# Performance work log

Hardware: AMD Instinct MI355X
Metric: run time of the kernel (lower is better)

## Reference

```python
import jax, jax.numpy as jnp
import numpy as np

B, S, D, E, K = 4, 4096, 1024, 8, 2


def setup_inputs() -> dict:
    key = jax.random.key(0)
    k0, k1, k2 = jax.random.split(key, 3)
    return {
        "x": jax.random.normal(k0, (B, S, D), dtype=jnp.float32),
        "gate_w": jax.random.normal(k1, (E, D), dtype=jnp.float32) * 0.02,   # torch Linear weight [out,in]
        "gate_b": jnp.zeros((E,), dtype=jnp.float32),
        "expert_w": jax.random.normal(k2, (E, D, D), dtype=jnp.float32) * 0.02,  # [E, out, in]
        "expert_b": jnp.zeros((E, D), dtype=jnp.float32),
    }


def reference(x, gate_w, gate_b, expert_w, expert_b):
    b, s, d = x.shape
    h = x.reshape(-1, d)                                   # [T, D], T = b*s
    # Router: gate linear -> softmax (float32) -> top-k -> renormalize
    router_logits = h @ gate_w.T + gate_b                  # [T, E]
    probs = jax.nn.softmax(router_logits.astype(jnp.float32), axis=-1)
    router_weights, selected_experts = jax.lax.top_k(probs, K)  # [T, K]
    router_weights = router_weights / router_weights.sum(axis=-1, keepdims=True)
    router_weights = router_weights.astype(h.dtype)
    # Combine weights per (token, expert): sum of top-k weights routed to each expert
    cw = (jax.nn.one_hot(selected_experts, E, dtype=h.dtype)
          * router_weights[..., None]).sum(axis=1)         # [T, E]
    # Dense-equivalent of gather-linear-scatter: every expert on every token,
    # then weighted combine (mathematically identical to the per-expert loop).
    expert_out = jnp.einsum('td,eod->teo', h, expert_w) + expert_b[None]  # [T, E, D]
    out = jnp.einsum('te,teo->to', cw, expert_out)         # [T, D]
    return out.reshape(b, s, d), router_logits, selected_experts
```

## Files before the change

### kernel.cpp

```cpp
#include <hip/hip_runtime.h>
#include <hip/hip_bf16.h>

#define T_TOK 16384
#define D_DIM 1024
#define E_EXP 8
#define NPAIR 28

#define BM 128
#define BN 128
#define BK 64

#define CNT_STRIDE 64

typedef __attribute__((ext_vector_type(4))) float f32x4;
typedef __attribute__((ext_vector_type(2))) float f32x2;
typedef __attribute__((ext_vector_type(8))) short bf16x8;
typedef __attribute__((ext_vector_type(4))) unsigned short u16x4;

static __device__ __forceinline__ unsigned short f2bf(float f) {
    unsigned int u = __float_as_uint(f);
    unsigned int r = 0x7FFFu + ((u >> 16) & 1u);
    return (unsigned short)((u + r) >> 16);
}

#define GLOAD_LDS16(gp, lp) \
    __builtin_amdgcn_global_load_lds( \
        (const __attribute__((address_space(1))) void*)(gp), \
        (__attribute__((address_space(3))) void*)(lp), 16, 0, 0)

__global__ __launch_bounds__(256) void convert_w_kernel(
    const float* __restrict__ w, unsigned short* __restrict__ o) {
    const int n4 = (E_EXP * D_DIM * D_DIM) / 4;
    for (int i = blockIdx.x * 256 + threadIdx.x; i < n4; i += gridDim.x * 256) {
        f32x4 v = ((const f32x4*)w)[i];
        u16x4 p;
        p[0] = f2bf(v[0]); p[1] = f2bf(v[1]); p[2] = f2bf(v[2]); p[3] = f2bf(v[3]);
        ((u16x4*)o)[i] = p;
    }
}

#define RTOK 64
__global__ __launch_bounds__(512) void router_kernel(
    const float* __restrict__ x, const float* __restrict__ gate_w,
    const float* __restrict__ gate_b, float* __restrict__ out_logits,
    float* __restrict__ out_sel, int* __restrict__ counts,
    int* __restrict__ pair_token, f32x2* __restrict__ pair_w,
    unsigned short* __restrict__ xbf) {
    __shared__ float gw[E_EXP][D_DIM];
    __shared__ float gb_s[E_EXP];
    __shared__ float logits_s[RTOK][E_EXP];
    __shared__ int   cnt_local[NPAIR];
    __shared__ int   gbase[NPAIR];
    __shared__ int   ent_p[RTOK];
    __shared__ int   ent_pos[RTOK];
    __shared__ f32x2 ent_w[RTOK];

    const int tid = threadIdx.x;
    for (int i = tid; i < E_EXP * D_DIM; i += 512) gw[0][i] = gate_w[i];
    if (tid < E_EXP) gb_s[tid] = gate_b[tid];
    if (tid < NPAIR) cnt_local[tid] = 0;
    __syncthreads();

    const int lane = tid & 63, wv = tid >> 6;
    for (int j = 0; j < RTOK / 8; ++j) {
        const int jt = wv * (RTOK / 8) + j;
        const int t = blockIdx.x * RTOK + jt;
        const float* xrow = x + (size_t)t * D_DIM;
        unsigned short* xbrow = xbf + (size_t)t * D_DIM;
        float acc[E_EXP] = {};
        #pragma unroll
        for (int c = 0; c < 4; ++c) {
            const int col = c * 256 + lane * 4;
            f32x4 xv = *(const f32x4*)(xrow + col);
            u16x4 pk;
            pk[0] = f2bf(xv[0]); pk[1] = f2bf(xv[1]); pk[2] = f2bf(xv[2]); pk[3] = f2bf(xv[3]);
            *(u16x4*)(xbrow + col) = pk;
            #pragma unroll
            for (int e = 0; e < E_EXP; ++e) {
                f32x4 gv = *(const f32x4*)(&gw[e][col]);
                acc[e] += xv[0] * gv[0] + xv[1] * gv[1] + xv[2] * gv[2] + xv[3] * gv[3];
            }
        }
        #pragma unroll
        for (int e = 0; e < E_EXP; ++e) {
            float v = acc[e];
            #pragma unroll
            for (int off = 32; off > 0; off >>= 1) v += __shfl_xor(v, off, 64);
            acc[e] = v;
        }
        if (lane == 0) {
            #pragma unroll
            for (int e = 0; e < E_EXP; ++e) logits_s[jt][e] = acc[e] + gb_s[e];
        }
    }
    __syncthreads();
    if (tid < RTOK) {
        const int t = blockIdx.x * RTOK + tid;
        float l[E_EXP], p[E_EXP];
        float m = -1e30f;
        #pragma unroll
        for (int e = 0; e < E_EXP; ++e) { l[e] = logits_s[tid][e]; m = fmaxf(m, l[e]); }
        float s = 0.f;
        #pragma unroll
        for (int e = 0; e < E_EXP; ++e) { p[e] = expf(l[e] - m); s += p[e]; }
        #pragma unroll
        for (int e = 0; e < E_EXP; ++e) p[e] /= s;
        int e0 = 0; float p0 = p[0];
        #pragma unroll
        for (int e = 1; e < E_EXP; ++e) if (p[e] > p0) { p0 = p[e]; e0 = e; }
        int e1 = -1; float p1 = -1e30f;
        #pragma unroll
        for (int e = 0; e < E_EXP; ++e) if (e != e0 && p[e] > p1) { p1 = p[e]; e1 = e; }
        float denom = p0 + p1;
        float w0 = p0 / denom, w1 = p1 / denom;
        out_sel[t * 2 + 0] = (float)e0;
        out_sel[t * 2 + 1] = (float)e1;
        int lo = min(e0, e1), hi = max(e0, e1);
        float wl = (e0 < e1) ? w0 : w1;
        float wh = (e0 < e1) ? w1 : w0;
        int pp = (lo * (15 - lo)) / 2 + (hi - lo - 1);
        int pos = atomicAdd(&cnt_local[pp], 1);
        ent_p[tid] = pp; ent_pos[tid] = pos;
        f32x2 wv2; wv2[0] = wl; wv2[1] = wh;
        ent_w[tid] = wv2;
    }
    __syncthreads();
    if (tid < NPAIR) gbase[tid] = atomicAdd(&counts[tid * CNT_STRIDE], cnt_local[tid]);
    if (tid < RTOK * E_EXP / 4) {
        f32x4 v = ((const f32x4*)&logits_s[0][0])[tid];
        ((f32x4*)(out_logits + (size_t)blockIdx.x * RTOK * E_EXP))[tid] = v;
    }
    __syncthreads();
    if (tid < RTOK) {
        int pp = ent_p[tid];
        int pos = gbase[pp] + ent_pos[tid];
        pair_token[pp * T_TOK + pos] = blockIdx.x * RTOK + tid;
        pair_w[pp * T_TOK + pos] = ent_w[tid];
    }
}

__global__ __launch_bounds__(256, 2) void moe_gemm_kernel(
    const unsigned short* __restrict__ xbf, const unsigned short* __restrict__ wbf,
    const float* __restrict__ expert_b, const int* __restrict__ counts,
    const int* __restrict__ pair_token, const f32x2* __restrict__ pair_w,
    float* __restrict__ out) {
    const int flat = blockIdx.x;
    const int cls = flat & 7;
    const int nt  = (flat >> 3) & 7;
    const int sup = flat >> 6;
    const int gidx = sup * 8 + cls;

    __shared__ int hdr[5];
    const int tid = threadIdx.x;
    if (tid < 64) {
        int c = (tid < NPAIR) ? counts[tid * CNT_STRIDE] : 0;
        int ntp = (c + BM - 1) >> 7;
        int s = ntp;
        #pragma unroll
        for (int off = 1; off < 64; off <<= 1) {
            int v = __shfl_up(s, off, 64);
            if (tid >= off) s += v;
        }
        int excl = s - ntp;
        bool mine = (tid < NPAIR) && (gidx >= excl) && (gidx < s);
        unsigned long long mb = __ballot(mine);
        int p = mb ? (__ffsll((long long)mb) - 1) : 0;
        int exclp = __shfl(excl, p, 64);
        int cp = __shfl(c, p, 64);
        if (tid == 0) {
            if (mb == 0) { hdr[0] = -1; }
            else {
                int lo = 0, q = p;
                while (q >= 7 - lo) { q -= 7 - lo; ++lo; }
                hdr[0] = lo; hdr[1] = lo + 1 + q;
                hdr[2] = (gidx - exclp) * BM; hdr[3] = cp; hdr[4] = p;
            }
        }
    }
    __syncthreads();
    const int lo = hdr[0];
    if (lo < 0) return;
    const int hi = hdr[1];
    const int m_base = hdr[2];
    const int cnt = hdr[3];
    const int p = hdr[4];
    const int n_base = nt * BN;

    __shared__ unsigned short As[BM * BK];
    __shared__ unsigned short B0s[BM * BK];
    __shared__ unsigned short B1s[BM * BK];
    __shared__ int tok_s[BM];
    __shared__ f32x2 w_s[BM];

    if (tid < BM) {
        int m = m_base + tid;
        int mc = (m < cnt) ? m : (cnt - 1);
        tok_s[tid] = pair_token[p * T_TOK + mc];
        w_s[tid]   = pair_w[p * T_TOK + mc];
    }
    __syncthreads();

    const int lane = tid & 63;
    const int w = tid >> 6;
    const int lr = lane & 15, lk = lane >> 4;
    const int wr = w >> 1, wc = w & 1;

    const int srow = lane >> 3;
    const int scol = 8 * ((lane & 7) ^ srow);
    const unsigned short* wb0 = wbf + ((size_t)lo << 20);
    const unsigned short* wb1 = wbf + ((size_t)hi << 20);
    const unsigned short* agp[4];
    const unsigned short* b0gp[4];
    const unsigned short* b1gp[4];
    int loff[4];
    #pragma unroll
    for (int i = 0; i < 4; ++i) {
        int R = i * 32 + w * 8 + srow;
        agp[i]  = xbf + (size_t)tok_s[R] * D_DIM + scol;
        b0gp[i] = wb0 + (size_t)(n_base + R) * D_DIM + scol;
        b1gp[i] = wb1 + (size_t)(n_base + R) * D_DIM + scol;
        loff[i] = (i * 32 + w * 8) * BK;
    }

    f32x4 acc0[4][4] = {};
    f32x4 acc1[4][4] = {};

    for (int k0 = 0; k0 < D_DIM; k0 += BK) {
        #pragma unroll
        for (int i = 0; i < 4; ++i) {
            GLOAD_LDS16(agp[i] + k0, &As[loff[i]]);
            GLOAD_LDS16(b0gp[i] + k0, &B0s[loff[i]]);
            GLOAD_LDS16(b1gp[i] + k0, &B1s[loff[i]]);
        }
        __syncthreads();
        #pragma unroll
        for (int kk = 0; kk < 2; ++kk) {
            bf16x8 a[4], b[4], c[4];
            #pragma unroll
            for (int m = 0; m < 4; ++m) {
                int R = wr * 64 + m * 16 + lr;
                int cb = (kk * 64 + lk * 16) ^ ((R & 7) << 4);
                a[m] = *(const bf16x8*)((const char*)As + R * 128 + cb);
            }
            #pragma unroll
            for (int n = 0; n < 4; ++n) {
                int R = wc * 64 + n * 16 + lr;
                int cb = (kk * 64 + lk * 16) ^ ((R & 7) << 4);
                b[n] = *(const bf16x8*)((const char*)B0s + R * 128 + cb);
            }
            #pragma unroll
            for (int m = 0; m < 4; ++m)
                #pragma unroll
                for (int n = 0; n < 4; ++n)
                    acc0[m][n] = __builtin_amdgcn_mfma_f32_16x16x32_bf16(a[m], b[n], acc0[m][n], 0, 0, 0);
            #pragma unroll
            for (int n = 0; n < 4; ++n) {
                int R = wc * 64 + n * 16 + lr;
                int cb = (kk * 64 + lk * 16) ^ ((R & 7) << 4);
                c[n] = *(const bf16x8*)((const char*)B1s + R * 128 + cb);
            }
            #pragma unroll
            for (int m = 0; m < 4; ++m)
                #pragma unroll
                for (int n = 0; n < 4; ++n)
                    acc1[m][n] = __builtin_amdgcn_mfma_f32_16x16x32_bf16(a[m], c[n], acc1[m][n], 0, 0, 0);
        }
        __syncthreads();
    }

    float blo[4], bhi[4];
    #pragma unroll
    for (int n = 0; n < 4; ++n) {
        int gn = n_base + wc * 64 + n * 16 + lr;
        blo[n] = expert_b[lo * D_DIM + gn];
        bhi[n] = expert_b[hi * D_DIM + gn];
    }
    #pragma unroll
    for (int m = 0; m < 4; ++m) {
        #pragma unroll
        for (int j = 0; j < 4; ++j) {
            int mi = wr * 64 + m * 16 + lk * 4 + j;
            if (m_base + mi >= cnt) continue;
            int tk = tok_s[mi];
            f32x2 wgt = w_s[mi];
            size_t obase = (size_t)tk * D_DIM + n_base + wc * 64 + lr;
            #pragma unroll
            for (int n = 0; n < 4; ++n)
                out[obase + n * 16] = wgt[0] * (acc0[m][n][j] + blo[n])
                                    + wgt[1] * (acc1[m][n][j] + bhi[n]);
        }
    }
}

extern "C" void kernel_launch(void* const* d_in, const int* in_sizes, int n_in,
                              void* d_out, int out_size, void* d_ws, size_t ws_size,
                              hipStream_t stream) {
    const float* x        = (const float*)d_in[0];
    const float* gate_w   = (const float*)d_in[1];
    const float* gate_b   = (const float*)d_in[2];
    const float* expert_w = (const float*)d_in[3];
    const float* expert_b = (const float*)d_in[4];

    float* out        = (float*)d_out;
    float* out_logits = out + (size_t)T_TOK * D_DIM;
    float* out_sel    = out_logits + (size_t)T_TOK * E_EXP;

    char* ws = (char*)d_ws;
    unsigned short* wbf = (unsigned short*)ws;
    unsigned short* xbf = (unsigned short*)(ws + 16777216);
    size_t off = 50331648;
    int*   counts     = (int*)(ws + off);
    int*   pair_token = (int*)(ws + off + 16384);
    f32x2* pair_w     = (f32x2*)(ws + off + 16384 + 1835008);

    hipMemsetAsync(counts, 0, NPAIR * CNT_STRIDE * sizeof(int), stream);

    convert_w_kernel<<<2048, 256, 0, stream>>>(expert_w, wbf);
    router_kernel<<<T_TOK / RTOK, 512, 0, stream>>>(x, gate_w, gate_b, out_logits,
                                                    out_sel, counts, pair_token,
                                                    pair_w, xbf);
    moe_gemm_kernel<<<20 * 64, 256, 0, stream>>>(xbf, wbf, expert_b, counts,
                                                 pair_token, pair_w, out);
}
```

Baseline: 134.7 us.

## Fuse weight conversion into router launch and double-buffer the MoE GEMM

The separate fp32-to-bf16 expert-weight conversion kernel is folded into the router launch as extra blocks, so conversion and routing run concurrently and one launch is removed. The grouped GEMM moves from 256 to 512 threads with an 8-wave 2x4 layout (smaller per-wave accumulator tiles) and double-buffered LDS. The next k-tile is prefetched while the current one computes, using explicit vmcnt waits, raw barriers and setprio around the MFMA bursts. LDS use doubles and occupancy drops to about one block per CU, and the hand-placed waitcnt/barrier scheme is fragile.

```diff
diff --git a/kernel.cpp b/kernel.cpp
--- a/kernel.cpp
+++ b/kernel.cpp
@@ -9,6 +9,7 @@
 #define BM 128
 #define BN 128
 #define BK 64
+#define NT_K (D_DIM / BK)
 
 #define CNT_STRIDE 64
 
@@ -28,24 +29,28 @@
         (const __attribute__((address_space(1))) void*)(gp), \
         (__attribute__((address_space(3))) void*)(lp), 16, 0, 0)
 
-__global__ __launch_bounds__(256) void convert_w_kernel(
-    const float* __restrict__ w, unsigned short* __restrict__ o) {
-    const int n4 = (E_EXP * D_DIM * D_DIM) / 4;
-    for (int i = blockIdx.x * 256 + threadIdx.x; i < n4; i += gridDim.x * 256) {
-        f32x4 v = ((const f32x4*)w)[i];
-        u16x4 p;
-        p[0] = f2bf(v[0]); p[1] = f2bf(v[1]); p[2] = f2bf(v[2]); p[3] = f2bf(v[3]);
-        ((u16x4*)o)[i] = p;
-    }
-}
-
 #define RTOK 64
-__global__ __launch_bounds__(512) void router_kernel(
+#define RBLK 256
+#define CBLK 128
+__global__ __launch_bounds__(512) void fused_router_kernel(
     const float* __restrict__ x, const float* __restrict__ gate_w,
     const float* __restrict__ gate_b, float* __restrict__ out_logits,
     float* __restrict__ out_sel, int* __restrict__ counts,
     int* __restrict__ pair_token, f32x2* __restrict__ pair_w,
-    unsigned short* __restrict__ xbf) {
+    unsigned short* __restrict__ xbf,
+    const float* __restrict__ expert_w, unsigned short* __restrict__ wbf) {
+    const int tid = threadIdx.x;
+    if (blockIdx.x >= RBLK) {
+        const int b = blockIdx.x - RBLK;
+        const int n4 = (E_EXP * D_DIM * D_DIM) / 4;
+        for (int i = b * 512 + tid; i < n4; i += CBLK * 512) {
+            f32x4 v = ((const f32x4*)expert_w)[i];
+            u16x4 p;
+            p[0] = f2bf(v[0]); p[1] = f2bf(v[1]); p[2] = f2bf(v[2]); p[3] = f2bf(v[3]);
+            ((u16x4*)wbf)[i] = p;
+        }
+        return;
+    }
     __shared__ float gw[E_EXP][D_DIM];
     __shared__ float gb_s[E_EXP];
     __shared__ float logits_s[RTOK][E_EXP];
@@ -55,7 +60,6 @@
     __shared__ int   ent_pos[RTOK];
     __shared__ f32x2 ent_w[RTOK];
 
-    const int tid = threadIdx.x;
     for (int i = tid; i < E_EXP * D_DIM; i += 512) gw[0][i] = gate_w[i];
     if (tid < E_EXP) gb_s[tid] = gate_b[tid];
     if (tid < NPAIR) cnt_local[tid] = 0;
@@ -139,7 +143,7 @@
     }
 }
 
-__global__ __launch_bounds__(256, 2) void moe_gemm_kernel(
+__global__ __launch_bounds__(512) void moe_gemm_kernel(
     const unsigned short* __restrict__ xbf, const unsigned short* __restrict__ wbf,
     const float* __restrict__ expert_b, const int* __restrict__ counts,
     const int* __restrict__ pair_token, const f32x2* __restrict__ pair_w,
@@ -186,9 +190,9 @@
     const int p = hdr[4];
     const int n_base = nt * BN;
 
-    __shared__ unsigned short As[BM * BK];
-    __shared__ unsigned short B0s[BM * BK];
-    __shared__ unsigned short B1s[BM * BK];
+    __shared__ unsigned short As[2][BM * BK];
+    __shared__ unsigned short B0s[2][BM * BK];
+    __shared__ unsigned short B1s[2][BM * BK];
     __shared__ int tok_s[BM];
     __shared__ f32x2 w_s[BM];
 
@@ -201,77 +205,89 @@
     __syncthreads();
 
     const int lane = tid & 63;
-    const int w = tid >> 6;
+    const int wv = tid >> 6;
+    const int wm = wv >> 2, wn = wv & 3;
     const int lr = lane & 15, lk = lane >> 4;
-    const int wr = w >> 1, wc = w & 1;
-
-    const int srow = lane >> 3;
-    const int scol = 8 * ((lane & 7) ^ srow);
+
+    const int r = tid >> 3;
+    const int swcol = 8 * ((tid & 7) ^ (r & 7));
     const unsigned short* wb0 = wbf + ((size_t)lo << 20);
     const unsigned short* wb1 = wbf + ((size_t)hi << 20);
-    const unsigned short* agp[4];
-    const unsigned short* b0gp[4];
-    const unsigned short* b1gp[4];
-    int loff[4];
+    const unsigned short* ag0  = xbf + (size_t)tok_s[r] * D_DIM + swcol;
+    const unsigned short* ag1  = xbf + (size_t)tok_s[64 + r] * D_DIM + swcol;
+    const unsigned short* b0g0 = wb0 + (size_t)(n_base + r) * D_DIM + swcol;
+    const unsigned short* b0g1 = wb0 + (size_t)(n_base + 64 + r) * D_DIM + swcol;
+    const unsigned short* b1g0 = wb1 + (size_t)(n_base + r) * D_DIM + swcol;
+    const unsigned short* b1g1 = wb1 + (size_t)(n_base + 64 + r) * D_DIM + swcol;
+    const int l0 = (wv * 64) * 8;
+    const int l1 = (512 + wv * 64) * 8;
+
+    f32x4 acc0[4][2] = {};
+    f32x4 acc1[4][2] = {};
+
+#define STAGE(buf, k0s) do { \
+        GLOAD_LDS16(ag0  + (k0s), &As[(buf)][l0]);  GLOAD_LDS16(ag1  + (k0s), &As[(buf)][l1]); \
+        GLOAD_LDS16(b0g0 + (k0s), &B0s[(buf)][l0]); GLOAD_LDS16(b0g1 + (k0s), &B0s[(buf)][l1]); \
+        GLOAD_LDS16(b1g0 + (k0s), &B1s[(buf)][l0]); GLOAD_LDS16(b1g1 + (k0s), &B1s[(buf)][l1]); \
+    } while (0)
+
+#define PHASE(buf, kk) do { \
+        const char* Ab = (const char*)&As[(buf)][0]; \
+        const char* Bb = (const char*)&B0s[(buf)][0]; \
+        const char* Cb = (const char*)&B1s[(buf)][0]; \
+        bf16x8 a[4], b[2], c[2]; \
+        _Pragma("unroll") \
+        for (int m = 0; m < 4; ++m) { \
+            int R = wm * 64 + m * 16 + lr; \
+            a[m] = *(const bf16x8*)(Ab + R * 128 + (((kk) * 64 + lk * 16) ^ ((R & 7) << 4))); \
+        } \
+        _Pragma("unroll") \
+        for (int n = 0; n < 2; ++n) { \
+            int R = wn * 32 + n * 16 + lr; \
+            int cb = ((kk) * 64 + lk * 16) ^ ((R & 7) << 4); \
+            b[n] = *(const bf16x8*)(Bb + R * 128 + cb); \
+            c[n] = *(const bf16x8*)(Cb + R * 128 + cb); \
+        } \
+        __builtin_amdgcn_s_setprio(1); \
+        _Pragma("unroll") \
+        for (int m = 0; m < 4; ++m) \
+            _Pragma("unroll") \
+            for (int n = 0; n < 2; ++n) \
+                acc0[m][n] = __builtin_amdgcn_mfma_f32_16x16x32_bf16(a[m], b[n], acc0[m][n], 0, 0, 0); \
+        _Pragma("unroll") \
+        for (int m = 0; m < 4; ++m) \
+            _Pragma("unroll") \
+            for (int n = 0; n < 2; ++n) \
+                acc1[m][n] = __builtin_amdgcn_mfma_f32_16x16x32_bf16(a[m], c[n], acc1[m][n], 0, 0, 0); \
+        __builtin_amdgcn_s_setprio(0); \
+    } while (0)
+
+    STAGE(0, 0);
+
+    #pragma unroll 1
+    for (int t = 0; t < NT_K - 1; ++t) {
+        const int buf = t & 1;
+        STAGE(buf ^ 1, (t + 1) * BK);
+        asm volatile("s_waitcnt vmcnt(6)" ::: "memory");
+        __builtin_amdgcn_s_barrier();
+        PHASE(buf, 0);
+        __builtin_amdgcn_s_barrier();
+        PHASE(buf, 1);
+        asm volatile("s_waitcnt lgkmcnt(0)" ::: "memory");
+        __builtin_amdgcn_s_barrier();
+    }
+    asm volatile("s_waitcnt vmcnt(0)" ::: "memory");
+    __builtin_amdgcn_s_barrier();
+    PHASE(1, 0);
+    __builtin_amdgcn_s_barrier();
+    PHASE(1, 1);
+#undef PHASE
+#undef STAGE
+
+    float blo[2], bhi[2];
     #pragma unroll
-    for (int i = 0; i < 4; ++i) {
-        int R = i * 32 + w * 8 + srow;
-        agp[i]  = xbf + (size_t)tok_s[R] * D_DIM + scol;
-        b0gp[i] = wb0 + (size_t)(n_base + R) * D_DIM + scol;
-        b1gp[i] = wb1 + (size_t)(n_base + R) * D_DIM + scol;
-        loff[i] = (i * 32 + w * 8) * BK;
-    }
-
-    f32x4 acc0[4][4] = {};
-    f32x4 acc1[4][4] = {};
-
-    for (int k0 = 0; k0 < D_DIM; k0 += BK) {
-        #pragma unroll
-        for (int i = 0; i < 4; ++i) {
-            GLOAD_LDS16(agp[i] + k0, &As[loff[i]]);
-            GLOAD_LDS16(b0gp[i] + k0, &B0s[loff[i]]);
-            GLOAD_LDS16(b1gp[i] + k0, &B1s[loff[i]]);
-        }
-        __syncthreads();
-        #pragma unroll
-        for (int kk = 0; kk < 2; ++kk) {
-            bf16x8 a[4], b[4], c[4];
-            #pragma unroll
-            for (int m = 0; m < 4; ++m) {
-                int R = wr * 64 + m * 16 + lr;
-                int cb = (kk * 64 + lk * 16) ^ ((R & 7) << 4);
-                a[m] = *(const bf16x8*)((const char*)As + R * 128 + cb);
-            }
-            #pragma unroll
-            for (int n = 0; n < 4; ++n) {
-                int R = wc * 64 + n * 16 + lr;
-                int cb = (kk * 64 + lk * 16) ^ ((R & 7) << 4);
-                b[n] = *(const bf16x8*)((const char*)B0s + R * 128 + cb);
-            }
-            #pragma unroll
-            for (int m = 0; m < 4; ++m)
-                #pragma unroll
-                for (int n = 0; n < 4; ++n)
-                    acc0[m][n] = __builtin_amdgcn_mfma_f32_16x16x32_bf16(a[m], b[n], acc0[m][n], 0, 0, 0);
-            #pragma unroll
-            for (int n = 0; n < 4; ++n) {
-                int R = wc * 64 + n * 16 + lr;
-                int cb = (kk * 64 + lk * 16) ^ ((R & 7) << 4);
-                c[n] = *(const bf16x8*)((const char*)B1s + R * 128 + cb);
-            }
-            #pragma unroll
-            for (int m = 0; m < 4; ++m)
-                #pragma unroll
-                for (int n = 0; n < 4; ++n)
-                    acc1[m][n] = __builtin_amdgcn_mfma_f32_16x16x32_bf16(a[m], c[n], acc1[m][n], 0, 0, 0);
-        }
-        __syncthreads();
-    }
-
-    float blo[4], bhi[4];
-    #pragma unroll
-    for (int n = 0; n < 4; ++n) {
-        int gn = n_base + wc * 64 + n * 16 + lr;
+    for (int n = 0; n < 2; ++n) {
+        int gn = n_base + wn * 32 + n * 16 + lr;
         blo[n] = expert_b[lo * D_DIM + gn];
         bhi[n] = expert_b[hi * D_DIM + gn];
     }
@@ -279,13 +295,13 @@
     for (int m = 0; m < 4; ++m) {
         #pragma unroll
         for (int j = 0; j < 4; ++j) {
-            int mi = wr * 64 + m * 16 + lk * 4 + j;
+            int mi = wm * 64 + m * 16 + lk * 4 + j;
             if (m_base + mi >= cnt) continue;
             int tk = tok_s[mi];
             f32x2 wgt = w_s[mi];
-            size_t obase = (size_t)tk * D_DIM + n_base + wc * 64 + lr;
+            size_t obase = (size_t)tk * D_DIM + n_base + wn * 32 + lr;
             #pragma unroll
-            for (int n = 0; n < 4; ++n)
+            for (int n = 0; n < 2; ++n)
                 out[obase + n * 16] = wgt[0] * (acc0[m][n][j] + blo[n])
                                     + wgt[1] * (acc1[m][n][j] + bhi[n]);
         }
@@ -315,10 +331,9 @@
 
     hipMemsetAsync(counts, 0, NPAIR * CNT_STRIDE * sizeof(int), stream);
 
-    convert_w_kernel<<<2048, 256, 0, stream>>>(expert_w, wbf);
-    router_kernel<<<T_TOK / RTOK, 512, 0, stream>>>(x, gate_w, gate_b, out_logits,
-                                                    out_sel, counts, pair_token,
-                                                    pair_w, xbf);
-    moe_gemm_kernel<<<20 * 64, 256, 0, stream>>>(xbf, wbf, expert_b, counts,
+    fused_router_kernel<<<RBLK + CBLK, 512, 0, stream>>>(
+        x, gate_w, gate_b, out_logits, out_sel, counts, pair_token, pair_w,
+        xbf, expert_w, wbf);
+    moe_gemm_kernel<<<20 * 64, 512, 0, stream>>>(xbf, wbf, expert_b, counts,
                                                  pair_token, pair_w, out);
 }
```

New measurement: 174.8 us. +29.8%, slower.
